# Optimization experiments

Hardware: AMD Instinct MI355X
Metric: run time of the kernel (lower is better)

Reference implementation:

```python
import jax, jax.numpy as jnp
import numpy as np
import math

HIDDEN = 512
NUM_HEADS = 8
HEAD_DIM = HIDDEN // NUM_HEADS
NUM_BUCKETS = 32
MAX_DISTANCE = 128


def _relative_position_bucket(rel_pos, bidirectional=True):
    # rel_pos: int32 [S, T]
    num_buckets = NUM_BUCKETS
    ret = 0
    if bidirectional:
        num_buckets //= 2
        ret = (rel_pos > 0).astype(jnp.int32) * num_buckets
        rel_pos = jnp.abs(rel_pos)
    else:
        rel_pos = -jnp.minimum(rel_pos, 0)
    max_exact = num_buckets // 2
    is_small = rel_pos < max_exact
    # guard log(0); result unused where is_small
    safe = jnp.maximum(rel_pos, 1).astype(jnp.float32)
    val_if_large = max_exact + (
        jnp.log(safe / max_exact) / math.log(MAX_DISTANCE / max_exact) * (num_buckets - max_exact)
    ).astype(jnp.int32)
    val_if_large = jnp.minimum(val_if_large, num_buckets - 1)
    return ret + jnp.where(is_small, rel_pos, val_if_large)


def setup_inputs() -> dict:
    key = jax.random.key(0)
    ks = jax.random.split(key, 6)
    B, S = 4, 2048
    std = 1.0 / math.sqrt(HIDDEN)
    inp = {
        "x": jax.random.normal(ks[0], (B, S, HIDDEN), dtype=jnp.float32),
        "Wq": jax.random.normal(ks[1], (HIDDEN, HIDDEN), dtype=jnp.float32) * std,
        "Wk": jax.random.normal(ks[2], (HIDDEN, HIDDEN), dtype=jnp.float32) * std,
        "Wv": jax.random.normal(ks[3], (HIDDEN, HIDDEN), dtype=jnp.float32) * std,
        "Wo": jax.random.normal(ks[4], (HIDDEN, HIDDEN), dtype=jnp.float32) * std,
        "bias_table": jax.random.normal(ks[5], (NUM_BUCKETS, NUM_HEADS), dtype=jnp.float32) * 0.02,
    }
    return inp


def reference(x, Wq, Wk, Wv, Wo, bias_table):
    # x: [B, S, HIDDEN]; weights: [HIDDEN, HIDDEN] (out = x @ W.T semantics folded as x @ W here
    # -- weights are random so orientation is a convention; we use x @ W).
    B, S, _ = x.shape
    T = S  # self-attention, context=None
    scale = HEAD_DIM ** -0.5

    def split_heads(t, L):
        return t.reshape(B, L, NUM_HEADS, HEAD_DIM).transpose(0, 2, 1, 3)  # [B,H,L,D]

    q = split_heads(x @ Wq, S)
    k = split_heads(x @ Wk, T)
    v = split_heads(x @ Wv, T)

    # relative position bias: [1, H, S, T]
    rel = jnp.arange(T, dtype=jnp.int32)[None, :] - jnp.arange(S, dtype=jnp.int32)[:, None]
    buckets = _relative_position_bucket(rel, bidirectional=True)  # [S, T]
    pos_bias = bias_table[buckets]  # [S, T, H]
    pos_bias = pos_bias.transpose(2, 0, 1)[None]  # [1, H, S, T]

    attn = jnp.einsum("bhsd,bhtd->bhst", q, k) * scale + pos_bias
    attn = jax.nn.softmax(attn, axis=-1)  # dropout = identity (eval)
    out = jnp.einsum("bhst,bhtd->bhsd", attn, v)
    out = out.transpose(0, 2, 1, 3).reshape(B, S, HIDDEN)
    return out @ Wo
```

## Files before the change

kernel.cpp:

```cpp
#include <hip/hip_runtime.h>
#include <hip/hip_bf16.h>
#include <math.h>

#define HIDDEN 512
#define NHEADS 8
#define HDIM 64
#define SLEN 2048
#define BATCH 4
#define NROWS (BATCH*SLEN)
#define RTAB (2*SLEN-1)
#define LOG2E 1.44269504088896340736f
#define SCALE_L2E (0.125f * LOG2E)

typedef _Float16 f16;
typedef f16 f16x8 __attribute__((ext_vector_type(8)));
typedef float f32x4 __attribute__((ext_vector_type(4)));
typedef unsigned short u16;
typedef unsigned int u32;
typedef u16 u16x4 __attribute__((ext_vector_type(4)));
typedef u16 u16x8 __attribute__((ext_vector_type(8)));
typedef u32 u32x4 __attribute__((ext_vector_type(4)));

__global__ __launch_bounds__(256) void prep(
    const float* __restrict__ x, const float* __restrict__ Wq,
    const float* __restrict__ Wk, const float* __restrict__ Wv,
    const float* __restrict__ Wo, const float* __restrict__ bias_table,
    u16* __restrict__ xh, u16* __restrict__ Wt, float* __restrict__ biasrel) {
  int bid = blockIdx.x;
  int tid = threadIdx.x;
  if (bid < 2048) {
    int i = bid * 256 + tid;
    const float4* p = (const float4*)(x + (size_t)i * 8);
    float4 a = p[0], b = p[1];
    u16x8 o;
    f16 t0 = (f16)a.x; o[0] = *(u16*)&t0;
    f16 t1 = (f16)a.y; o[1] = *(u16*)&t1;
    f16 t2 = (f16)a.z; o[2] = *(u16*)&t2;
    f16 t3 = (f16)a.w; o[3] = *(u16*)&t3;
    f16 t4 = (f16)b.x; o[4] = *(u16*)&t4;
    f16 t5 = (f16)b.y; o[5] = *(u16*)&t5;
    f16 t6 = (f16)b.z; o[6] = *(u16*)&t6;
    f16 t7 = (f16)b.w; o[7] = *(u16*)&t7;
    *(u16x8*)(xh + (size_t)i * 8) = o;
  } else if (bid < 2560) {
    int wb = bid - 2048;
    int wy = wb >> 7;
    const float* W = wy == 0 ? Wq : wy == 1 ? Wk : wy == 2 ? Wv : Wo;
    u16* dst = Wt + (size_t)wy * HIDDEN * HIDDEN;
    int t = (wb & 127) * 256 + tid;
    int k = t >> 6, n0 = (t & 63) << 3;
    const float4* p = (const float4*)(W + (size_t)k * HIDDEN + n0);
    float4 a = p[0], b = p[1];
    float vals[8] = {a.x, a.y, a.z, a.w, b.x, b.y, b.z, b.w};
#pragma unroll
    for (int j = 0; j < 8; ++j) {
      f16 hv = (f16)vals[j];
      dst[(size_t)(n0 + j) * HIDDEN + k] = *(u16*)&hv;
    }
  } else {
    int i = (bid - 2560) * 256 + tid;
    if (i >= NHEADS * RTAB) return;
    int h = i / RTAB;
    int idx = i - h * RTAB;
    int rel = idx - (SLEN - 1);
    int ret = rel > 0 ? 16 : 0;
    int a = rel < 0 ? -rel : rel;
    int bidx;
    if (a < 8) {
      bidx = a;
    } else {
      float val = logf((float)a * 0.125f) / logf(16.0f) * 8.0f;
      bidx = 8 + (int)val;
      if (bidx > 15) bidx = 15;
    }
    biasrel[i] = bias_table[(ret + bidx) * NHEADS + h] * LOG2E;
  }
}

__global__ __launch_bounds__(256) void gemm_mfma(
    const u16* __restrict__ A, const u16* __restrict__ Wt0,
    const u16* __restrict__ Wt1, const u16* __restrict__ Wt2,
    void* __restrict__ O, int mode) {
  __shared__ u16 sm[2 * 128 * 72];
  u16 (*As)[72] = (u16(*)[72])sm;
  u16 (*Bs)[72] = (u16(*)[72])(sm + 128 * 72);
  const u16* Wt = blockIdx.z == 0 ? Wt0 : blockIdx.z == 1 ? Wt1 : Wt2;
  const int tid = threadIdx.x;
  const int w = tid >> 6, l = tid & 63;
  const int lr = l & 15, lg = l >> 4;
  const int wr = w >> 1, wc = w & 1;
  const int m0 = blockIdx.x << 7, n0 = blockIdx.y << 7;
  const int vtmode = (mode == 1) && (blockIdx.z == 2);

  f32x4 acc[4][4] = {};

  u16x8 areg[4], breg[4];
#pragma unroll
  for (int e = 0; e < 4; ++e) {
    int c = (e << 8) + tid;
    int row = c >> 3, g = c & 7;
    areg[e] = *(const u16x8*)(A + (size_t)(m0 + row) * HIDDEN + (g << 3));
    breg[e] = *(const u16x8*)(Wt + (size_t)(n0 + row) * HIDDEN + (g << 3));
  }

  for (int k0 = 0; k0 < HIDDEN; k0 += 64) {
    __syncthreads();
#pragma unroll
    for (int e = 0; e < 4; ++e) {
      int c = (e << 8) + tid;
      int row = c >> 3, g = c & 7;
      *(u16x8*)&As[row][g << 3] = areg[e];
      *(u16x8*)&Bs[row][g << 3] = breg[e];
    }
    __syncthreads();
    if (k0 + 64 < HIDDEN) {
#pragma unroll
      for (int e = 0; e < 4; ++e) {
        int c = (e << 8) + tid;
        int row = c >> 3, g = c & 7;
        areg[e] = *(const u16x8*)(A + (size_t)(m0 + row) * HIDDEN + k0 + 64 + (g << 3));
        breg[e] = *(const u16x8*)(Wt + (size_t)(n0 + row) * HIDDEN + k0 + 64 + (g << 3));
      }
    }
#pragma unroll
    for (int kk = 0; kk < 64; kk += 32) {
      f16x8 af[4], bf[4];
#pragma unroll
      for (int mt = 0; mt < 4; ++mt)
        af[mt] = *(const f16x8*)&As[(wr << 6) + (mt << 4) + lr][kk + (lg << 3)];
#pragma unroll
      for (int nt = 0; nt < 4; ++nt)
        bf[nt] = *(const f16x8*)&Bs[(wc << 6) + (nt << 4) + lr][kk + (lg << 3)];
      if (!vtmode) {
#pragma unroll
        for (int mt = 0; mt < 4; ++mt)
#pragma unroll
          for (int nt = 0; nt < 4; ++nt)
            acc[mt][nt] = __builtin_amdgcn_mfma_f32_16x16x32_f16(
                af[mt], bf[nt], acc[mt][nt], 0, 0, 0);
      } else {
#pragma unroll
        for (int i = 0; i < 4; ++i)
#pragma unroll
          for (int j = 0; j < 4; ++j)
            acc[i][j] = __builtin_amdgcn_mfma_f32_16x16x32_f16(
                bf[i], af[j], acc[i][j], 0, 0, 0);
      }
    }
  }

  if (mode == 0) {
    float* Of = (float*)O;
#pragma unroll
    for (int mt = 0; mt < 4; ++mt)
#pragma unroll
      for (int nt = 0; nt < 4; ++nt)
#pragma unroll
        for (int r = 0; r < 4; ++r) {
          int m = m0 + (wr << 6) + (mt << 4) + (lg << 2) + r;
          int n = n0 + (wc << 6) + (nt << 4) + lr;
          Of[(size_t)m * HIDDEN + n] = acc[mt][nt][r];
        }
  } else if (!vtmode) {
    __syncthreads();
    u16* tt = sm;
    const float osc = (blockIdx.z == 0) ? SCALE_L2E : 1.0f;
#pragma unroll
    for (int mt = 0; mt < 4; ++mt)
#pragma unroll
      for (int nt = 0; nt < 4; ++nt)
#pragma unroll
        for (int r = 0; r < 4; ++r) {
          int ml = (wr << 6) + (mt << 4) + (lg << 2) + r;
          int nl = (wc << 6) + (nt << 4) + lr;
          f16 hv = (f16)(acc[mt][nt][r] * osc);
          tt[ml * 136 + nl] = *(u16*)&hv;
        }
    __syncthreads();
    u16* O16 = (u16*)O + (size_t)blockIdx.z * NROWS * HIDDEN;
    int b = m0 >> 11, s0 = m0 & (SLEN - 1);
    int hl = tid >> 7, rr = tid & 127;
    int hh = (n0 >> 6) + hl;
    u16* obase = O16 + (((size_t)b * NHEADS + hh) * SLEN + s0) * HDIM;
#pragma unroll
    for (int c = 0; c < 8; ++c) {
      int sl = (rr >> 3) + (c << 4);
      int d8 = (rr & 7) << 3;
      u16x8 v = *(const u16x8*)&tt[sl * 136 + (hl << 6) + d8];
      *(u16x8*)(obase + (size_t)sl * HDIM + d8) = v;
    }
  } else {
    __syncthreads();
    u16* tt = sm;
#pragma unroll
    for (int i = 0; i < 4; ++i)
#pragma unroll
      for (int j = 0; j < 4; ++j)
#pragma unroll
        for (int r = 0; r < 4; ++r) {
          int nl = (wc << 6) + (i << 4) + (lg << 2) + r;
          int ml = (wr << 6) + (j << 4) + lr;
          f16 hv = (f16)acc[i][j][r];
          tt[nl * 136 + ml] = *(u16*)&hv;
        }
    __syncthreads();
    u16* O16 = (u16*)O + (size_t)2 * NROWS * HIDDEN;
    int nl = tid >> 1, half = tid & 1;
    int n = n0 + nl;
    int h = n >> 6, d = n & 63;
    int b = m0 >> 11, s_base = m0 & (SLEN - 1);
    u16* orow = O16 + (((size_t)b * NHEADS + h) * HDIM + d) * SLEN + s_base;
    const u16* trow = tt + nl * 136;
#pragma unroll
    for (int c = 0; c < 8; ++c) {
      int v_off = (half << 6) + (c << 3);
      int c0 = (v_off & ~31) | (((v_off >> 3) & 3) << 2);
      u16x4 lo = *(const u16x4*)(trow + c0);
      u16x4 hi = *(const u16x4*)(trow + c0 + 16);
      u16x8 st;
#pragma unroll
      for (int j = 0; j < 4; ++j) { st[j] = lo[j]; st[j + 4] = hi[j]; }
      *(u16x8*)(orow + v_off) = st;
    }
  }
}

__global__ __launch_bounds__(256, 4) void flash_attn_mfma(
    const u16* __restrict__ qg, const u16* __restrict__ kg,
    const u16* __restrict__ vtg, const float* __restrict__ biasrel,
    u16* __restrict__ attn_out) {
  __shared__ u16 Ks[2][64][72];
  __shared__ u16 Vt[2][64][72];

  const int tid = threadIdx.x;
  const int w = tid >> 6, l = tid & 63;
  const int lr = l & 15, lg = l >> 4;

  int bid = blockIdx.x;
  int xcd = bid & 7, idx = bid >> 3;
  int bh = (xcd << 2) + (idx >> 5);
  int bx = idx & 31;
  int h = bh & 7, b = bh >> 3;
  int q0 = bx << 6;

  const u16* qp = qg + (size_t)bh * (SLEN * HDIM);
  const u16* kp = kg + (size_t)bh * (SLEN * HDIM);
  const u16* vp = vtg + (size_t)bh * (HDIM * SLEN);

  const float bias_pos = biasrel[h * RTAB + 2 * (SLEN - 1)];
  const float bias_neg = biasrel[h * RTAB];

  f16x8 aq0, aq1;
  {
    const u16* qrow = qp + (size_t)(q0 + (w << 4) + lr) * HDIM + (lg << 3);
    aq0 = *(const f16x8*)(qrow);
    aq1 = *(const f16x8*)(qrow + 32);
  }

  const float* bb = biasrel + h * RTAB + (SLEN - 1) + (lg << 2) - lr - q0 - (w << 4);

  f32x4 acc[4] = {};
  f32x4 accl = {};
  const f16x8 ones = {(f16)1.f, (f16)1.f, (f16)1.f, (f16)1.f,
                      (f16)1.f, (f16)1.f, (f16)1.f, (f16)1.f};

  u16x8 kreg[2], vreg[2];
#pragma unroll
  for (int e = 0; e < 2; ++e) {
    int c = tid + (e << 8);
    int row = c >> 3, c8 = (c & 7) << 3;
    kreg[e] = *(const u16x8*)(kp + (size_t)row * HDIM + c8);
    vreg[e] = *(const u16x8*)(vp + (size_t)row * SLEN + c8);
  }
#pragma unroll
  for (int e = 0; e < 2; ++e) {
    int c = tid + (e << 8);
    int row = c >> 3, c8 = (c & 7) << 3;
    *(u16x8*)&Ks[0][row][c8] = kreg[e];
    *(u16x8*)&Vt[0][row][c8] = vreg[e];
  }
#pragma unroll
  for (int e = 0; e < 2; ++e) {
    int c = tid + (e << 8);
    int row = c >> 3, c8 = (c & 7) << 3;
    kreg[e] = *(const u16x8*)(kp + (size_t)(64 + row) * HDIM + c8);
    vreg[e] = *(const u16x8*)(vp + (size_t)row * SLEN + 64 + c8);
  }
  __syncthreads();

  int cur = 0;
  for (int t0 = 0; t0 < SLEN; t0 += 64) {
    if (t0 + 64 < SLEN) {
#pragma unroll
      for (int e = 0; e < 2; ++e) {
        int c = tid + (e << 8);
        int row = c >> 3, c8 = (c & 7) << 3;
        *(u16x8*)&Ks[cur ^ 1][row][c8] = kreg[e];
        *(u16x8*)&Vt[cur ^ 1][row][c8] = vreg[e];
      }
      if (t0 + 128 < SLEN) {
#pragma unroll
        for (int e = 0; e < 2; ++e) {
          int c = tid + (e << 8);
          int row = c >> 3, c8 = (c & 7) << 3;
          kreg[e] = *(const u16x8*)(kp + (size_t)(t0 + 128 + row) * HDIM + c8);
          vreg[e] = *(const u16x8*)(vp + (size_t)row * SLEN + t0 + 128 + c8);
        }
      }
    }

    int dtq = t0 - q0;
    f32x4 sc[4];
    if (dtq >= 192 || dtq <= -192) {
      float c = (dtq > 0) ? bias_pos : bias_neg;
      f32x4 cv = {c, c, c, c};
#pragma unroll
      for (int ct = 0; ct < 4; ++ct) sc[ct] = cv;
    } else {
#pragma unroll
      for (int ct = 0; ct < 4; ++ct)
#pragma unroll
        for (int r = 0; r < 4; ++r)
          sc[ct][r] = bb[t0 + (ct << 4) + r];
    }

    f16x8 kf[4][2];
#pragma unroll
    for (int ct = 0; ct < 4; ++ct) {
      kf[ct][0] = *(const f16x8*)&Ks[cur][(ct << 4) + lr][lg << 3];
      kf[ct][1] = *(const f16x8*)&Ks[cur][(ct << 4) + lr][32 + (lg << 3)];
    }

    __builtin_amdgcn_s_setprio(1);
#pragma unroll
    for (int ct = 0; ct < 4; ++ct) {
      sc[ct] = __builtin_amdgcn_mfma_f32_16x16x32_f16(
          kf[ct][0], aq0, sc[ct], 0, 0, 0);
      sc[ct] = __builtin_amdgcn_mfma_f32_16x16x32_f16(
          kf[ct][1], aq1, sc[ct], 0, 0, 0);
    }
    __builtin_amdgcn_s_setprio(0);

#pragma unroll
    for (int ct = 0; ct < 4; ++ct)
#pragma unroll
      for (int r = 0; r < 4; ++r)
        sc[ct][r] = __builtin_amdgcn_exp2f(sc[ct][r]);

    f16x8 vf[2][4];
#pragma unroll
    for (int kb = 0; kb < 2; ++kb)
#pragma unroll
      for (int dt = 0; dt < 4; ++dt)
        vf[kb][dt] = *(const f16x8*)&Vt[cur][(dt << 4) + lr][(kb << 5) + (lg << 3)];

    __builtin_amdgcn_s_setprio(1);
#pragma unroll
    for (int kb = 0; kb < 2; ++kb) {
      u32 a0 = __builtin_bit_cast(u32,
          __builtin_amdgcn_cvt_pkrtz(sc[2 * kb][0], sc[2 * kb][1]));
      u32 a1 = __builtin_bit_cast(u32,
          __builtin_amdgcn_cvt_pkrtz(sc[2 * kb][2], sc[2 * kb][3]));
      u32 a2 = __builtin_bit_cast(u32,
          __builtin_amdgcn_cvt_pkrtz(sc[2 * kb + 1][0], sc[2 * kb + 1][1]));
      u32 a3 = __builtin_bit_cast(u32,
          __builtin_amdgcn_cvt_pkrtz(sc[2 * kb + 1][2], sc[2 * kb + 1][3]));
      u32x4 pk = {a0, a1, a2, a3};
      f16x8 pa = __builtin_bit_cast(f16x8, pk);
      accl = __builtin_amdgcn_mfma_f32_16x16x32_f16(pa, ones, accl, 0, 0, 0);
#pragma unroll
      for (int dt = 0; dt < 4; ++dt)
        acc[dt] = __builtin_amdgcn_mfma_f32_16x16x32_f16(
            pa, vf[kb][dt], acc[dt], 0, 0, 0);
    }
    __builtin_amdgcn_s_setprio(0);

    __syncthreads();
    cur ^= 1;
  }

  {
    float linv[4];
#pragma unroll
    for (int r = 0; r < 4; ++r) linv[r] = 1.f / accl[r];
    u16* op = attn_out +
              ((size_t)(b * SLEN) + q0 + (w << 4)) * HIDDEN + (h << 6);
#pragma unroll
    for (int r = 0; r < 4; ++r)
#pragma unroll
      for (int dt = 0; dt < 4; ++dt) {
        f16 hv = (f16)(acc[dt][r] * linv[r]);
        op[(size_t)((lg << 2) + r) * HIDDEN + (dt << 4) + lr] = *(u16*)&hv;
      }
  }
}

extern "C" void kernel_launch(void* const* d_in, const int* in_sizes, int n_in,
                              void* d_out, int out_size, void* d_ws, size_t ws_size,
                              hipStream_t stream) {
  const float* x          = (const float*)d_in[0];
  const float* Wq         = (const float*)d_in[1];
  const float* Wk         = (const float*)d_in[2];
  const float* Wv         = (const float*)d_in[3];
  const float* Wo         = (const float*)d_in[4];
  const float* bias_table = (const float*)d_in[5];
  float* out = (float*)d_out;

  u16* xh   = (u16*)d_ws;
  u16* wt   = xh + (size_t)NROWS * HIDDEN;
  u16* qkv  = wt + (size_t)4 * HIDDEN * HIDDEN;
  u16* attno_h = qkv + (size_t)3 * NROWS * HIDDEN;
  float* biasrel = (float*)(attno_h + (size_t)NROWS * HIDDEN);

  u16* qb = qkv;
  u16* kb = qkv + (size_t)NROWS * HIDDEN;
  u16* vb = qkv + (size_t)2 * NROWS * HIDDEN;

  prep<<<2688, 256, 0, stream>>>(x, Wq, Wk, Wv, Wo, bias_table, xh, wt, biasrel);

  u16* wtq = wt;
  u16* wtk = wt + (size_t)HIDDEN * HIDDEN;
  u16* wtv = wt + (size_t)2 * HIDDEN * HIDDEN;
  u16* wto = wt + (size_t)3 * HIDDEN * HIDDEN;

  gemm_mfma<<<dim3(NROWS / 128, HIDDEN / 128, 3), 256, 0, stream>>>(
      xh, wtq, wtk, wtv, qkv, 1);

  flash_attn_mfma<<<SLEN / 64 * BATCH * NHEADS, 256, 0, stream>>>(
      qb, kb, vb, biasrel, attno_h);

  gemm_mfma<<<dim3(NROWS / 128, HIDDEN / 128, 1), 256, 0, stream>>>(
      attno_h, wto, wto, wto, out, 0);
}
```

Measured before the change: 108.9 us.

## Double attention query tile to 128 rows with 512-thread blocks

Flash attention blocks now cover 128 query rows with 8 waves instead of 64 rows with 4 waves. The 64-row K/V tile is shared by twice as many query rows, which halves global K/V traffic per query. Each thread now loads a single K/V chunk per tile, and the constant-bias skip threshold is adjusted for the larger query window. The trade-off is half as many blocks and a larger block size that may limit occupancy; the unseen output-write code must also handle the new wave count correctly.

```diff
diff --git a/kernel.cpp b/kernel.cpp
--- a/kernel.cpp
+++ b/kernel.cpp
@@ -225,7 +225,7 @@
   }
 }
 
-__global__ __launch_bounds__(256, 4) void flash_attn_mfma(
+__global__ __launch_bounds__(512, 4) void flash_attn_mfma(
     const u16* __restrict__ qg, const u16* __restrict__ kg,
     const u16* __restrict__ vtg, const float* __restrict__ biasrel,
     u16* __restrict__ attn_out) {
@@ -238,10 +238,10 @@
 
   int bid = blockIdx.x;
   int xcd = bid & 7, idx = bid >> 3;
-  int bh = (xcd << 2) + (idx >> 5);
-  int bx = idx & 31;
+  int bh = (xcd << 2) + (idx >> 4);
+  int bx = idx & 15;
   int h = bh & 7, b = bh >> 3;
-  int q0 = bx << 6;
+  int q0 = bx << 7;
 
   const u16* qp = qg + (size_t)bh * (SLEN * HDIM);
   const u16* kp = kg + (size_t)bh * (SLEN * HDIM);
@@ -264,54 +264,33 @@
   const f16x8 ones = {(f16)1.f, (f16)1.f, (f16)1.f, (f16)1.f,
                       (f16)1.f, (f16)1.f, (f16)1.f, (f16)1.f};
 
-  u16x8 kreg[2], vreg[2];
-#pragma unroll
-  for (int e = 0; e < 2; ++e) {
-    int c = tid + (e << 8);
-    int row = c >> 3, c8 = (c & 7) << 3;
-    kreg[e] = *(const u16x8*)(kp + (size_t)row * HDIM + c8);
-    vreg[e] = *(const u16x8*)(vp + (size_t)row * SLEN + c8);
-  }
-#pragma unroll
-  for (int e = 0; e < 2; ++e) {
-    int c = tid + (e << 8);
-    int row = c >> 3, c8 = (c & 7) << 3;
-    *(u16x8*)&Ks[0][row][c8] = kreg[e];
-    *(u16x8*)&Vt[0][row][c8] = vreg[e];
-  }
-#pragma unroll
-  for (int e = 0; e < 2; ++e) {
-    int c = tid + (e << 8);
-    int row = c >> 3, c8 = (c & 7) << 3;
-    kreg[e] = *(const u16x8*)(kp + (size_t)(64 + row) * HDIM + c8);
-    vreg[e] = *(const u16x8*)(vp + (size_t)row * SLEN + 64 + c8);
+  u16x8 kreg, vreg;
+  {
+    int row = tid >> 3, c8 = (tid & 7) << 3;
+    kreg = *(const u16x8*)(kp + (size_t)row * HDIM + c8);
+    vreg = *(const u16x8*)(vp + (size_t)row * SLEN + c8);
+    *(u16x8*)&Ks[0][row][c8] = kreg;
+    *(u16x8*)&Vt[0][row][c8] = vreg;
+    kreg = *(const u16x8*)(kp + (size_t)(64 + row) * HDIM + c8);
+    vreg = *(const u16x8*)(vp + (size_t)row * SLEN + 64 + c8);
   }
   __syncthreads();
 
   int cur = 0;
   for (int t0 = 0; t0 < SLEN; t0 += 64) {
     if (t0 + 64 < SLEN) {
-#pragma unroll
-      for (int e = 0; e < 2; ++e) {
-        int c = tid + (e << 8);
-        int row = c >> 3, c8 = (c & 7) << 3;
-        *(u16x8*)&Ks[cur ^ 1][row][c8] = kreg[e];
-        *(u16x8*)&Vt[cur ^ 1][row][c8] = vreg[e];
-      }
+      int row = tid >> 3, c8 = (tid & 7) << 3;
+      *(u16x8*)&Ks[cur ^ 1][row][c8] = kreg;
+      *(u16x8*)&Vt[cur ^ 1][row][c8] = vreg;
       if (t0 + 128 < SLEN) {
-#pragma unroll
-        for (int e = 0; e < 2; ++e) {
-          int c = tid + (e << 8);
-          int row = c >> 3, c8 = (c & 7) << 3;
-          kreg[e] = *(const u16x8*)(kp + (size_t)(t0 + 128 + row) * HDIM + c8);
-          vreg[e] = *(const u16x8*)(vp + (size_t)row * SLEN + t0 + 128 + c8);
-        }
+        kreg = *(const u16x8*)(kp + (size_t)(t0 + 128 + row) * HDIM + c8);
+        vreg = *(const u16x8*)(vp + (size_t)row * SLEN + t0 + 128 + c8);
       }
     }
 
     int dtq = t0 - q0;
     f32x4 sc[4];
-    if (dtq >= 192 || dtq <= -192) {
+    if (dtq >= 256 || dtq <= -192) {
       float c = (dtq > 0) ? bias_pos : bias_neg;
       f32x4 cv = {c, c, c, c};
 #pragma unroll
@@ -426,7 +405,7 @@
   gemm_mfma<<<dim3(NROWS / 128, HIDDEN / 128, 3), 256, 0, stream>>>(
       xh, wtq, wtk, wtv, qkv, 1);
 
-  flash_attn_mfma<<<SLEN / 64 * BATCH * NHEADS, 256, 0, stream>>>(
+  flash_attn_mfma<<<SLEN / 128 * BATCH * NHEADS, 512, 0, stream>>>(
       qb, kb, vb, biasrel, attno_h);
 
   gemm_mfma<<<dim3(NROWS / 128, HIDDEN / 128, 1), 256, 0, stream>>>(
```

New measurement: 101.8 us. 1.07x faster.
